# Optimization experiments

Measured on AMD Instinct MI355X. Metric: run time of the kernel, lower is better.

The kernel has to match this reference:

```python
import jax, jax.numpy as jnp
import numpy as np

PS = 7  # window size
HEADS = 8


def setup_inputs() -> dict:
    key = jax.random.key(0)
    ks = jax.random.split(key, 5)
    b, C, H, W = 2, 384, 224, 224
    x = jax.random.normal(ks[0], (b, C, H, W), dtype=jnp.float32)
    # Conv2d(dim, 3*dim, k=1, bias=False) -> weight [3C, C]
    qkv_w = jax.random.normal(ks[1], (3 * C, C), dtype=jnp.float32) * (1.0 / np.sqrt(C))
    # depthwise Conv2d(3*dim, 3*dim, k=3, groups=3*dim) -> weight [3C, 1, 3, 3]
    dw_w = jax.random.normal(ks[2], (3 * C, 1, 3, 3), dtype=jnp.float32) * (1.0 / 3.0)
    # temperature parameter, initialized to ones like the module
    temperature = jnp.ones((HEADS, 1, 1), dtype=jnp.float32)
    # Conv2d(dim, dim, k=1, bias=False) -> weight [C, C]
    proj_w = jax.random.normal(ks[3], (C, C), dtype=jnp.float32) * (1.0 / np.sqrt(C))
    return {"x": x, "qkv_w": qkv_w, "dw_w": dw_w, "temperature": temperature, "proj_w": proj_w}


def _l2norm(t):
    n = jnp.sqrt(jnp.sum(t * t, axis=-1, keepdims=True))
    return t / jnp.maximum(n, 1e-12)  # matches F.normalize semantics


def reference(x, qkv_w, dw_w, temperature, proj_w):
    b, C, H, W = x.shape
    heads, ps = HEADS, PS
    d = C // heads
    nh, nw = H // ps, W // ps

    # 1x1 conv qkv projection (pointwise -> einsum)
    qkv = jnp.einsum('bchw,oc->bohw', x, qkv_w)
    # depthwise 3x3 conv, padding=1
    qkv = jax.lax.conv_general_dilated(
        qkv, dw_w, window_strides=(1, 1), padding='SAME',
        feature_group_count=3 * C, dimension_numbers=('NCHW', 'OIHW', 'NCHW'))
    q, k, v = jnp.split(qkv, 3, axis=1)

    def to_win(t):
        # b (head d) (nh ps) (nw ps) -> b (nh nw) head d (ps ps)
        t = t.reshape(b, heads, d, nh, ps, nw, ps)
        t = t.transpose(0, 3, 5, 1, 2, 4, 6)
        return t.reshape(b, nh * nw, heads, d, ps * ps)

    q, k, v = to_win(q), to_win(k), to_win(v)
    q = _l2norm(q)
    k = _l2norm(k)

    # channel-transposed attention: d x d scores per window
    attn = jnp.einsum('bwhds,bwhes->bwhde', q, k) * temperature
    attn = jax.nn.softmax(attn, axis=-1)
    out = jnp.einsum('bwhde,bwhes->bwhds', attn, v)

    # inverse rearrange: b (nh nw) head d (ps ps) -> b (head d) (nh ps) (nw ps)
    out = out.reshape(b, nh, nw, heads, d, ps, ps)
    out = out.transpose(0, 3, 4, 1, 5, 2, 6).reshape(b, C, H, W)

    return jnp.einsum('bchw,oc->bohw', out, proj_w)
```

## Files before the change

### kernel.cpp

```cpp
#include <hip/hip_runtime.h>


#define NB     2
#define CC     384
#define C3     1152
#define HH     224
#define WW2    224
#define HW     50176
#define NHEADS 8
#define DD     48
#define PSZ    7
#define NWINS  1024
#define SS     49
#define SSP    50
#define WS50   (NWINS*SSP)

typedef unsigned int  u32;
typedef unsigned short u16;
typedef __bf16 bf16x8 __attribute__((ext_vector_type(8)));
typedef float  f32x4  __attribute__((ext_vector_type(4)));

__device__ __forceinline__ u16 f2bf(float f){
  union { __bf16 h; u16 u; } v; v.h = (__bf16)f; return v.u;
}
__device__ __forceinline__ float bf2f(u16 h){
  union { u32 u; float f; } v; v.u = ((u32)h) << 16;
  return v.f;
}
__device__ __forceinline__ float u16lo(u32 u){
  union { u32 u; float f; } v; v.u = u << 16; return v.f;
}
__device__ __forceinline__ float u16hi(u32 u){
  union { u32 u; float f; } v; v.u = u & 0xffff0000u; return v.f;
}

typedef __attribute__((address_space(3))) u32 as3_u32;
typedef __attribute__((address_space(1))) const u32 as1_u32;
__device__ __forceinline__ void gld16(const void* g, void* l){
  __builtin_amdgcn_global_load_lds((as1_u32*)(unsigned long long)(g),
                                   (as3_u32*)(u32)(unsigned long long)(l),
                                   16, 0, 0);
}

__device__ __forceinline__ int xcdswz(int bid, int cpx){
  return (bid & 7)*cpx + (bid >> 3);
}

__device__ __forceinline__ int swz(int row, int col){
  return row*64 + (col ^ ((row & 7) << 3));
}

__global__ void k_cvt(const float* __restrict__ qw, const float* __restrict__ pw,
                      u16* __restrict__ qwb, u16* __restrict__ pwb){
  int i = blockIdx.x * 256 + threadIdx.x;
  if (i < C3*CC) qwb[i] = f2bf(qw[i]);
  if (i < CC*CC) pwb[i] = f2bf(pw[i]);
}

__global__ void k_sentinel(float* __restrict__ out, int n){
  int i = blockIdx.x * 256 + threadIdx.x;
  if (i < n) out[i] = 12345.0f;
}

#define CPAD 386
__global__ __launch_bounds__(256) void k_trx(const float* __restrict__ x,
                                             u16* __restrict__ xt){
  const int pt = blockIdx.x, b = blockIdx.y, tid = threadIdx.x;
  __shared__ u16 t[64*CPAD];
  const float* xb = x + (size_t)b*CC*HW + pt*64;
  #pragma unroll
  for (int it=0; it<24; ++it){
    int i = tid + it*256;
    int c = i >> 4, p4 = (i & 15)*4;
    float4 v = *(const float4*)(xb + (size_t)c*HW + p4);
    t[(p4+0)*CPAD + c] = f2bf(v.x);
    t[(p4+1)*CPAD + c] = f2bf(v.y);
    t[(p4+2)*CPAD + c] = f2bf(v.z);
    t[(p4+3)*CPAD + c] = f2bf(v.w);
  }
  __syncthreads();
  u32* dst = (u32*)(xt + ((size_t)b*HW + (size_t)pt*64)*CC);
  #pragma unroll
  for (int it=0; it<48; ++it){
    int j = tid + it*256;
    int p = j / 192, c2 = j - p*192;
    dst[j] = *(const u32*)(t + p*CPAD + c2*2);
  }
}

template<int OUT_F32, int MT, int CPX>
__global__ __launch_bounds__(256) void k_gemm(const u16* __restrict__ A,
    const u16* __restrict__ B, void* __restrict__ Cdst){
  __shared__ __align__(16) u16 As[128*32];
  __shared__ __align__(16) u16 Bs[128*32];
  const int wg = xcdswz(blockIdx.x, CPX);
  const int m0 = (wg % MT) * 128;
  const int t1 = wg / MT;
  const int n0 = (t1 % 392) * 128;
  const int b  = t1 / 392;
  const int M  = MT * 128;
  const int tid = threadIdx.x, lane = tid & 63, wv = tid >> 6;
  const int wm = (wv & 1) * 64, wn = (wv >> 1) * 64;
  const int lr = lane & 15, lg = lane >> 4;
  const u16* Bb = B + (size_t)b*HW*CC;

  f32x4 acc[4][4];
  #pragma unroll
  for (int i=0;i<4;++i)
    #pragma unroll
    for (int j=0;j<4;++j) acc[i][j] = {0.f,0.f,0.f,0.f};

  for (int kk=0; kk<12; ++kk){
    const int k0 = kk*32;
    __syncthreads();
    #pragma unroll
    for (int i=0;i<2;++i){
      int chunk = i*256 + tid;
      int row = chunk >> 2, c4 = chunk & 3;
      gld16(A  + (size_t)(m0+row)*CC + k0 + c4*8, As + chunk*8);
      gld16(Bb + (size_t)(n0+row)*CC + k0 + c4*8, Bs + chunk*8);
    }
    __syncthreads();
    bf16x8 af[4], bfr[4];
    #pragma unroll
    for (int i=0;i<4;++i) af[i]  = *(const bf16x8*)(As + (wm + i*16 + lr)*32 + lg*8);
    #pragma unroll
    for (int j=0;j<4;++j) bfr[j] = *(const bf16x8*)(Bs + (wn + j*16 + lr)*32 + lg*8);
    #pragma unroll
    for (int i=0;i<4;++i)
      #pragma unroll
      for (int j=0;j<4;++j)
        acc[i][j] = __builtin_amdgcn_mfma_f32_16x16x32_bf16(af[i], bfr[j], acc[i][j], 0, 0, 0);
  }
  #pragma unroll
  for (int i=0;i<4;++i){
    #pragma unroll
    for (int j=0;j<4;++j){
      const int row = m0 + wm + i*16 + lg*4;
      const int col = n0 + wn + j*16 + lr;
      if (OUT_F32){
        float* Cp = (float*)Cdst + (size_t)b*M*HW;
        #pragma unroll
        for (int r=0;r<4;++r) Cp[(size_t)(row+r)*HW + col] = acc[i][j][r];
      } else {
        u16* Cp = (u16*)Cdst + (size_t)b*M*HW;
        #pragma unroll
        for (int r=0;r<4;++r) Cp[(size_t)(row+r)*HW + col] = f2bf(acc[i][j][r]);
      }
    }
  }
}

#define DWL 240
__global__ __launch_bounds__(128) void k_dw(const u16* __restrict__ qkv,
    const float* __restrict__ dww, u16* __restrict__ qkv2){
  const int wg = xcdswz(blockIdx.x, 2304);
  const int wy = wg & 31;
  const int t1 = wg >> 5;
  const int o0 = (t1 % 288) * 4;
  const int b  = t1 / 288;
  const int tid = threadIdx.x;
  __shared__ __align__(16) u16 lin[4*9*DWL];
  __shared__ __align__(16) u16 outb[4*32*SSP];

  const int y0 = wy*PSZ - 1;

  if (tid < 72){
    int ch = tid/18, rem = tid%18, r = rem>>1;
    lin[ch*9*DWL + r*DWL + ((rem&1) ? 232 : 7)] = 0;
  }
  outb[tid*SSP + 49] = 0;

  #pragma unroll
  for (int it=0; it<8; ++it){
    int i = tid + it*128;
    if (i < 1008){
      int ch = i / 252, rem = i - ch*252;
      int r = rem / 28, c16 = rem - r*28;
      int y = y0 + r;
      uint4 v = {0,0,0,0};
      if (y >= 0 && y < HH)
        v = *(const uint4*)(qkv + (size_t)(b*C3 + o0 + ch)*HW + (size_t)y*WW2 + c16*8);
      *(uint4*)(lin + ch*9*DWL + r*DWL + 8 + c16*8) = v;
    }
  }
  __syncthreads();

  {
    const int ch = tid >> 5, wx = tid & 31;
    const u16* L = lin + ch*9*DWL;
    const int xb = wx*PSZ;
    const int s0 = (xb+7) & ~1;
    const bool par = (xb+7) & 1;

    float wk[9];
    #pragma unroll
    for (int i=0;i<9;++i) wk[i] = dww[(o0+ch)*9 + i];

    float tr[3][9];
    #define LOADROW(slot, r) {                                   \
      u32 u0 = *(const u32*)(L + (r)*DWL + s0);                  \
      u32 u1 = *(const u32*)(L + (r)*DWL + s0 + 2);              \
      u32 u2 = *(const u32*)(L + (r)*DWL + s0 + 4);              \
      u32 u3 = *(const u32*)(L + (r)*DWL + s0 + 6);              \
      u32 u4 = *(const u32*)(L + (r)*DWL + s0 + 8);              \
      float a0=u16lo(u0),a1=u16hi(u0),a2=u16lo(u1),a3=u16hi(u1); \
      float a4=u16lo(u2),a5=u16hi(u2),a6=u16lo(u3),a7=u16hi(u3); \
      float a8=u16lo(u4),a9=u16hi(u4);                           \
      tr[slot][0]=par?a1:a0; tr[slot][1]=par?a2:a1;              \
      tr[slot][2]=par?a3:a2; tr[slot][3]=par?a4:a3;              \
      tr[slot][4]=par?a5:a4; tr[slot][5]=par?a6:a5;              \
      tr[slot][6]=par?a7:a6; tr[slot][7]=par?a8:a7;              \
      tr[slot][8]=par?a9:a8; }

    LOADROW(0, 0)
    LOADROW(1, 1)

    u32 pk[24];
    u16 last;
    #pragma unroll
    for (int pi=0; pi<7; ++pi){
      LOADROW((pi+2)%3, pi+2)
      const float* r0 = tr[pi%3];
      const float* r1 = tr[(pi+1)%3];
      const float* r2 = tr[(pi+2)%3];
      float o[7];
      #pragma unroll
      for (int pj=0; pj<7; ++pj){
        float s = 0.f;
        #pragma unroll
        for (int kx=0;kx<3;++kx){
          s += wk[kx]  *r0[pj+kx];
          s += wk[3+kx]*r1[pj+kx];
          s += wk[6+kx]*r2[pj+kx];
        }
        o[pj] = s;
      }
      #pragma unroll
      for (int pj=0; pj<7; ++pj){
        int idx = pi*7 + pj;
        u16 bv = f2bf(o[pj]);
        if (idx == 48){ last = bv; }
        else {
          if ((idx & 1) == 0) pk[idx>>1] = (u32)bv;
          else                pk[idx>>1] |= ((u32)bv) << 16;
        }
      }
    }
    u16* rec = outb + tid*SSP;
    #pragma unroll
    for (int i=0;i<24;++i) *(u32*)(rec + 2*i) = pk[i];
    rec[48] = last;
  }
  __syncthreads();

  #pragma unroll
  for (int it=0; it<7; ++it){
    int i = tid + it*128;
    if (i < 800){
      int ch = i / 200, idx = i - ch*200;
      u16* dst = qkv2 + ((size_t)(b*C3 + o0 + ch)*NWINS + (size_t)wy*32)*SSP;
      *(uint4*)(dst + idx*8) = *(const uint4*)(outb + ch*32*SSP + idx*8);
    }
  }
}

__global__ __launch_bounds__(256) void k_attn(const u16* __restrict__ qkv2,
    const float* __restrict__ temp, u16* __restrict__ aout){
  const int h = blockIdx.x, win = blockIdx.y, b = blockIdx.z;
  const int tid = threadIdx.x, lane = tid & 63, wv = tid >> 6;
  const int lr = lane & 15, lg = lane >> 4;

  __shared__ __align__(16) u16 q_s[48*64], k_s[48*64], v_t[64*64], p_s[48*64];
  __shared__ float invq[48], invk[48];

  for (int i=tid; i<48*32; i+=256){ ((u32*)q_s)[i]=0u; ((u32*)k_s)[i]=0u; ((u32*)p_s)[i]=0u; }
  for (int i=tid; i<64*32; i+=256) ((u32*)v_t)[i]=0u;
  __syncthreads();

  const u16* qsrc = qkv2 + ((size_t)(b*C3 +        h*DD)*NWINS + win)*SSP;
  const u16* ksrc = qkv2 + ((size_t)(b*C3 + CC   + h*DD)*NWINS + win)*SSP;
  const u16* vsrc = qkv2 + ((size_t)(b*C3 + 2*CC + h*DD)*NWINS + win)*SSP;
  for (int i=tid; i<48*25; i+=256){
    int dc = i / 25, c = i - dc*25;
    size_t off = (size_t)dc*WS50 + 2*c;
    u32 vq = *(const u32*)(qsrc + off);
    u32 vk = *(const u32*)(ksrc + off);
    u32 vv = *(const u32*)(vsrc + off);
    int sw = swz(dc, 2*c);
    *(u32*)(q_s + sw) = vq;
    *(u32*)(k_s + sw) = vk;
    v_t[swz(2*c,   dc)] = (u16)(vv & 0xffffu);
    v_t[swz(2*c+1, dc)] = (u16)(vv >> 16);
  }
  __syncthreads();

  if (tid < 192){
    const int row96 = tid >> 1, half = tid & 1;
    const int rr = (row96 < 48) ? row96 : row96 - 48;
    const u16* a = (row96 < 48) ? q_s : k_s;
    const int s0 = half ? 25 : 0, s1 = half ? 49 : 25;
    float sum = 0.f;
    for (int s=s0; s<s1; ++s){ float v = bf2f(a[swz(rr,s)]); sum += v*v; }
    sum += __shfl_xor(sum, 1);
    if (!half){
      float inv = 1.f / fmaxf(sqrtf(sum), 1e-12f);
      if (row96 < 48) invq[rr] = inv * temp[h]; else invk[rr] = inv;
    }
  }
  __syncthreads();

  if (wv < 3){
    const int ti = wv;
    f32x4 c3[3];
    #pragma unroll
    for (int tj=0;tj<3;++tj) c3[tj] = {0.f,0.f,0.f,0.f};
    #pragma unroll
    for (int tj=0;tj<3;++tj){
      #pragma unroll
      for (int ks=0; ks<2; ++ks){
        bf16x8 a  = *(const bf16x8*)(q_s + swz(ti*16+lr, ks*32 + lg*8));
        bf16x8 bb = *(const bf16x8*)(k_s + swz(tj*16+lr, ks*32 + lg*8));
        c3[tj] = __builtin_amdgcn_mfma_f32_16x16x32_bf16(a, bb, c3[tj], 0,0,0);
      }
    }
    const float ik0 = invk[lr], ik1 = invk[16+lr], ik2 = invk[32+lr];
    #pragma unroll
    for (int r=0;r<4;++r){
      const int row = ti*16 + lg*4 + r;
      const float iq = invq[row];
      float l0 = c3[0][r]*iq*ik0, l1 = c3[1][r]*iq*ik1, l2 = c3[2][r]*iq*ik2;
      float m = fmaxf(fmaxf(l0,l1),l2);
      m = fmaxf(m, __shfl_xor(m,1)); m = fmaxf(m, __shfl_xor(m,2));
      m = fmaxf(m, __shfl_xor(m,4)); m = fmaxf(m, __shfl_xor(m,8));
      float e0 = __expf(l0-m), e1 = __expf(l1-m), e2 = __expf(l2-m);
      float s = e0+e1+e2;
      s += __shfl_xor(s,1); s += __shfl_xor(s,2);
      s += __shfl_xor(s,4); s += __shfl_xor(s,8);
      const float is = 1.f / s;
      p_s[swz(row, lr)]    = f2bf(e0*is);
      p_s[swz(row, 16+lr)] = f2bf(e1*is);
      p_s[swz(row, 32+lr)] = f2bf(e2*is);
    }
  }
  __syncthreads();

  const int wy = win >> 5, wx = win & 31;
  u16* ab = aout + (size_t)b*HW*CC + (size_t)h*DD;
  for (int t = wv; t < 12; t += 4){
    int ti = t >> 2, tj = t & 3;
    f32x4 c = {0.f,0.f,0.f,0.f};
    #pragma unroll
    for (int ks=0; ks<2; ++ks){
      bf16x8 a  = *(const bf16x8*)(p_s + swz(ti*16+lr, ks*32 + lg*8));
      bf16x8 bb = *(const bf16x8*)(v_t + swz(tj*16+lr, ks*32 + lg*8));
      c = __builtin_amdgcn_mfma_f32_16x16x32_bf16(a, bb, c, 0,0,0);
    }
    int scol = tj*16 + lr;
    if (scol < SS){
      int pi = scol / PSZ, pj = scol - pi*PSZ;
      size_t p = (size_t)(wy*PSZ + pi)*WW2 + wx*PSZ + pj;
      u32 lo = (u32)f2bf(c[0]) | ((u32)f2bf(c[1]) << 16);
      u32 hi = (u32)f2bf(c[2]) | ((u32)f2bf(c[3]) << 16);
      u32* dst = (u32*)(ab + p*CC + ti*16 + lg*4);
      dst[0] = lo; dst[1] = hi;
    }
  }
}

extern "C" void kernel_launch(void* const* d_in, const int* in_sizes, int n_in,
                              void* d_out, int out_size, void* d_ws, size_t ws_size,
                              hipStream_t stream) {
  const float* x     = (const float*)d_in[0];
  const float* qkvw  = (const float*)d_in[1];
  const float* dww   = (const float*)d_in[2];
  const float* temp  = (const float*)d_in[3];
  const float* projw = (const float*)d_in[4];
  float* out = (float*)d_out;

  const size_t SZ_QKV   = (size_t)NB*C3*HW*2;
  const size_t SZ_QKV2  = (size_t)NB*C3*NWINS*SSP*2;
  const size_t OFF_QKV2 = SZ_QKV;
  const size_t OFF_W1   = OFF_QKV2 + SZ_QKV2;
  const size_t OFF_W2   = OFF_W1 + (size_t)C3*CC*2;
  const size_t NEEDED   = OFF_W2 + (size_t)CC*CC*2;

  if (ws_size < NEEDED){
    k_sentinel<<<(out_size + 255)/256, 256, 0, stream>>>(out, out_size);
    return;
  }
  char* ws = (char*)d_ws;
  u16* qkv  = (u16*)ws;
  u16* qkv2 = (u16*)(ws + OFF_QKV2);
  u16* xt   = (u16*)(ws + OFF_QKV2);
  u16* ao   = (u16*)ws;
  u16* qwb  = (u16*)(ws + OFF_W1);
  u16* pwb  = (u16*)(ws + OFF_W2);

  k_cvt<<<dim3((C3*CC)/256), 256, 0, stream>>>(qkvw, projw, qwb, pwb);
  k_trx<<<dim3(784, NB), 256, 0, stream>>>(x, xt);
  k_gemm<0,9,882><<<dim3(7056), 256, 0, stream>>>(qwb, xt, qkv);
  k_dw<<<dim3(18432), 128, 0, stream>>>(qkv, dww, qkv2);
  k_attn<<<dim3(NHEADS, NWINS, NB), 256, 0, stream>>>(qkv2, temp, ao);
  k_gemm<1,3,294><<<dim3(2352), 256, 0, stream>>>(pwb, ao, out);
}
```

Baseline: 558.6 us.

## Double-buffer GEMM LDS tiles with BK=64 and XOR-swizzled layout

Rewrites the 1x1-conv GEMM main loop to use two LDS buffers of 128x64 tiles. The next K-slice is loaded while the current one is computed, which halves the barrier count and overlaps global loads with MFMA work. An XOR swizzle on the 16-byte column chunks is added to reduce LDS bank conflicts on the fragment reads. LDS use per block rises to 64 KB, which may lower occupancy.

```diff
diff --git a/kernel.cpp b/kernel.cpp
--- a/kernel.cpp
+++ b/kernel.cpp
@@ -91,8 +91,8 @@
 template<int OUT_F32, int MT, int CPX>
 __global__ __launch_bounds__(256) void k_gemm(const u16* __restrict__ A,
     const u16* __restrict__ B, void* __restrict__ Cdst){
-  __shared__ __align__(16) u16 As[128*32];
-  __shared__ __align__(16) u16 Bs[128*32];
+  __shared__ __align__(16) u16 As0[128*64], Bs0[128*64];
+  __shared__ __align__(16) u16 As1[128*64], Bs1[128*64];
   const int wg = xcdswz(blockIdx.x, CPX);
   const int m0 = (wg % MT) * 128;
   const int t1 = wg / MT;
@@ -110,28 +110,49 @@
     #pragma unroll
     for (int j=0;j<4;++j) acc[i][j] = {0.f,0.f,0.f,0.f};
 
-  for (int kk=0; kk<12; ++kk){
-    const int k0 = kk*32;
+  const int srow[4] = { (tid+  0)>>3, (tid+256)>>3, (tid+512)>>3, (tid+768)>>3 };
+  const int sc8  = tid & 7;
+
+  #define STAGE(AD, BD, K0) {                                             \
+    _Pragma("unroll")                                                     \
+    for (int i=0;i<4;++i){                                                \
+      int row = srow[i];                                                  \
+      int csrc = sc8 ^ (row & 7);                                         \
+      gld16(A  + (size_t)(m0+row)*CC + (K0) + csrc*8, AD + (i*256+tid)*8);\
+      gld16(Bb + (size_t)(n0+row)*CC + (K0) + csrc*8, BD + (i*256+tid)*8);\
+    } }
+
+  #define COMPUTE(AD, BD) {                                               \
+    _Pragma("unroll")                                                     \
+    for (int ks=0; ks<2; ++ks){                                           \
+      const int cp = (((ks*4 + lg) ^ (lr & 7)) << 3);                     \
+      bf16x8 af[4], bfr[4];                                               \
+      _Pragma("unroll")                                                   \
+      for (int i=0;i<4;++i) af[i]  = *(const bf16x8*)(AD + (wm + i*16 + lr)*64 + cp); \
+      _Pragma("unroll")                                                   \
+      for (int j=0;j<4;++j) bfr[j] = *(const bf16x8*)(BD + (wn + j*16 + lr)*64 + cp); \
+      _Pragma("unroll")                                                   \
+      for (int i=0;i<4;++i)                                               \
+        _Pragma("unroll")                                                 \
+        for (int j=0;j<4;++j)                                             \
+          acc[i][j] = __builtin_amdgcn_mfma_f32_16x16x32_bf16(af[i], bfr[j], acc[i][j], 0, 0, 0); \
+    } }
+
+  STAGE(As0, Bs0, 0)
+  __syncthreads();
+  #pragma unroll
+  for (int kk2=0; kk2<3; ++kk2){
+    const int k0 = kk2*128;
+    if (kk2*2+1 < 6) STAGE(As1, Bs1, k0+64)
+    COMPUTE(As0, Bs0)
     __syncthreads();
-    #pragma unroll
-    for (int i=0;i<2;++i){
-      int chunk = i*256 + tid;
-      int row = chunk >> 2, c4 = chunk & 3;
-      gld16(A  + (size_t)(m0+row)*CC + k0 + c4*8, As + chunk*8);
-      gld16(Bb + (size_t)(n0+row)*CC + k0 + c4*8, Bs + chunk*8);
-    }
+    if (kk2*2+2 < 6) STAGE(As0, Bs0, k0+128)
+    COMPUTE(As1, Bs1)
     __syncthreads();
-    bf16x8 af[4], bfr[4];
-    #pragma unroll
-    for (int i=0;i<4;++i) af[i]  = *(const bf16x8*)(As + (wm + i*16 + lr)*32 + lg*8);
-    #pragma unroll
-    for (int j=0;j<4;++j) bfr[j] = *(const bf16x8*)(Bs + (wn + j*16 + lr)*32 + lg*8);
-    #pragma unroll
-    for (int i=0;i<4;++i)
-      #pragma unroll
-      for (int j=0;j<4;++j)
-        acc[i][j] = __builtin_amdgcn_mfma_f32_16x16x32_bf16(af[i], bfr[j], acc[i][j], 0, 0, 0);
-  }
+  }
+  #undef STAGE
+  #undef COMPUTE
+
   #pragma unroll
   for (int i=0;i<4;++i){
     #pragma unroll
```

Result: faster. 545.1 us (-2.4%).
